# Kernel optimization log

Hardware: AMD Instinct MI355X
Metric: run time of the kernel (lower is better)

The kernel has to match this reference:

```python
import jax, jax.numpy as jnp
import numpy as np

VV = 100000   # value vocab
VP = 100000   # path vocab
VT = 50257    # tag vocab
E = 128       # embedding size
B = 2048      # batch of functions
N = 10        # rep_size (contexts per function)


def setup_inputs() -> dict:
    key = jax.random.key(0)
    ks = jax.random.split(key, 10)
    return {
        "value1_idx": jax.random.randint(ks[0], (B, N), 0, VV),
        "path_idx": jax.random.randint(ks[1], (B, N), 0, VP),
        "value2_idx": jax.random.randint(ks[2], (B, N), 0, VV),
        "value_emb": jax.random.normal(ks[3], (VV, E), jnp.float32) * 0.02,
        "path_emb": jax.random.normal(ks[4], (VP, E), jnp.float32) * 0.02,
        "tag_emb": jax.random.normal(ks[5], (VT, E), jnp.float32) * 0.02,
        "W_fc": jax.random.normal(ks[6], (3 * E, E), jnp.float32) * 0.02,
        "b_fc": jnp.zeros((E,), jnp.float32),
        "w_att": jax.random.normal(ks[7], (E,), jnp.float32) * 0.02,
        "b_att": jnp.zeros((), jnp.float32),
    }


def reference(value1_idx, path_idx, value2_idx, value_emb, path_emb, tag_emb,
              W_fc, b_fc, w_att, b_att):
    # Per-context embedding gathers: [B, N, E]
    v1 = value_emb[value1_idx]
    p = path_emb[path_idx]
    v2 = value_emb[value2_idx]
    ctx = jnp.concatenate([v1, p, v2], axis=-1)          # [B, N, 3E]
    c_tilde = jnp.tanh(ctx @ W_fc + b_fc)                # [B, N, E]
    # Attention pooling over the N contexts
    att = jax.nn.softmax(c_tilde @ w_att + b_att, axis=1)  # [B, N]
    v = jnp.einsum('bne,bn->be', c_tilde, att)           # [B, E]
    # Softmax classifier over all tags
    logits = v @ tag_emb.T                               # [B, VT]
    q = jax.nn.softmax(logits, axis=-1)
    return q
```

## Files before the change

### kernel.cpp

```cpp
#include <hip/hip_runtime.h>
#include <hip/hip_bf16.h>
#include <math.h>

#define VTAG 50257
#define EDIM 128
#define NREP 10
#define BFUNC 2048
#define NSTRIP 786
#define NPAD (NSTRIP * 64)

typedef __bf16 bf16x8 __attribute__((ext_vector_type(8)));
typedef float f32x4 __attribute__((ext_vector_type(4)));

__device__ __forceinline__ unsigned short f2bf(float x) {
    unsigned u = __float_as_uint(x);
    unsigned r = (u + 0x7fffu + ((u >> 16) & 1u)) >> 16;
    return (unsigned short)r;
}

__global__ __launch_bounds__(128) void k1_attn(
    const int* __restrict__ v1i, const int* __restrict__ pti,
    const int* __restrict__ v2i,
    const float* __restrict__ vemb, const float* __restrict__ pemb,
    const float* __restrict__ Wfc, const float* __restrict__ bfc,
    const float* __restrict__ watt, const float* __restrict__ batt,
    unsigned short* __restrict__ vbf)
{
    const int b = blockIdx.x;
    const int e = threadIdx.x;
    __shared__ float ctx[NREP][3 * EDIM];
    __shared__ float red[2][NREP];

    #pragma unroll
    for (int j = 0; j < 30; ++j) {
        int i = j * 128 + e;
        int n = i / 384;
        int c = i - n * 384;
        float val;
        if (c < 128)      val = vemb[(size_t)v1i[b * NREP + n] * EDIM + c];
        else if (c < 256) val = pemb[(size_t)pti[b * NREP + n] * EDIM + (c - 128)];
        else              val = vemb[(size_t)v2i[b * NREP + n] * EDIM + (c - 256)];
        ctx[n][c] = val;
    }
    __syncthreads();

    float acc[NREP];
    #pragma unroll
    for (int n = 0; n < NREP; ++n) acc[n] = 0.f;

    for (int k = 0; k < 384; k += 4) {
        float w0 = Wfc[(k + 0) * EDIM + e];
        float w1 = Wfc[(k + 1) * EDIM + e];
        float w2 = Wfc[(k + 2) * EDIM + e];
        float w3 = Wfc[(k + 3) * EDIM + e];
        #pragma unroll
        for (int n = 0; n < NREP; ++n) {
            float4 c4 = *(const float4*)&ctx[n][k];
            acc[n] = fmaf(c4.x, w0, acc[n]);
            acc[n] = fmaf(c4.y, w1, acc[n]);
            acc[n] = fmaf(c4.z, w2, acc[n]);
            acc[n] = fmaf(c4.w, w3, acc[n]);
        }
    }

    const float bias = bfc[e];
    const float we = watt[e];
    float ct[NREP];
    #pragma unroll
    for (int n = 0; n < NREP; ++n) ct[n] = tanhf(acc[n] + bias);

    const int wv = e >> 6, ln = e & 63;
    #pragma unroll
    for (int n = 0; n < NREP; ++n) {
        float p = ct[n] * we;
        p += __shfl_xor(p, 32);
        p += __shfl_xor(p, 16);
        p += __shfl_xor(p, 8);
        p += __shfl_xor(p, 4);
        p += __shfl_xor(p, 2);
        p += __shfl_xor(p, 1);
        if (ln == 0) red[wv][n] = p;
    }
    __syncthreads();

    const float batt0 = batt[0];
    float al[NREP];
    float m = -1e30f;
    #pragma unroll
    for (int n = 0; n < NREP; ++n) {
        al[n] = red[0][n] + red[1][n] + batt0;
        m = fmaxf(m, al[n]);
    }
    float s = 0.f;
    #pragma unroll
    for (int n = 0; n < NREP; ++n) { al[n] = __expf(al[n] - m); s += al[n]; }
    const float inv = 1.f / s;

    float v = 0.f;
    #pragma unroll
    for (int n = 0; n < NREP; ++n) v = fmaf(al[n] * inv, ct[n], v);

    vbf[b * EDIM + e] = f2bf(v);
}

__global__ __launch_bounds__(256) void k_conv_tag(
    const float* __restrict__ tag, unsigned short* __restrict__ tbf)
{
    size_t i = ((size_t)blockIdx.x * 256 + threadIdx.x) * 4;
    if (i >= (size_t)NPAD * EDIM) return;
    float4 x = make_float4(0.f, 0.f, 0.f, 0.f);
    if (i < (size_t)VTAG * EDIM) x = *(const float4*)(tag + i);
    ushort4 o;
    o.x = f2bf(x.x); o.y = f2bf(x.y); o.z = f2bf(x.z); o.w = f2bf(x.w);
    *(ushort4*)(tbf + i) = o;
}

__global__ __launch_bounds__(256) void k2_partial(
    const unsigned short* __restrict__ vbf, const unsigned short* __restrict__ tbf,
    float* __restrict__ psumT)
{
    const int wave = threadIdx.x >> 6;
    const int lane = threadIdx.x & 63;
    const int quad = lane >> 4;
    const int l16  = lane & 15;
    const int strip = blockIdx.y;
    const int n0 = strip * 64;
    const int rowbase = blockIdx.x * 128 + wave * 32;

    __shared__ float srow[128];

    const bf16x8* tb8 = (const bf16x8*)tbf;
    const bf16x8* vb8 = (const bf16x8*)vbf;

    bf16x8 bfrag[4][4];
    #pragma unroll
    for (int nt = 0; nt < 4; ++nt) {
        int col = n0 + nt * 16 + l16;
        const bf16x8* p = tb8 + (size_t)col * 16 + quad;
        #pragma unroll
        for (int ks = 0; ks < 4; ++ks) bfrag[nt][ks] = p[ks * 4];
    }
    bf16x8 afrag[2][4];
    #pragma unroll
    for (int mt = 0; mt < 2; ++mt) {
        int row = rowbase + mt * 16 + l16;
        const bf16x8* p = vb8 + (size_t)row * 16 + quad;
        #pragma unroll
        for (int ks = 0; ks < 4; ++ks) afrag[mt][ks] = p[ks * 4];
    }

    f32x4 acc[2][4];
    #pragma unroll
    for (int mt = 0; mt < 2; ++mt)
        #pragma unroll
        for (int nt = 0; nt < 4; ++nt) acc[mt][nt] = (f32x4){0.f, 0.f, 0.f, 0.f};

    #pragma unroll
    for (int ks = 0; ks < 4; ++ks)
        #pragma unroll
        for (int mt = 0; mt < 2; ++mt)
            #pragma unroll
            for (int nt = 0; nt < 4; ++nt)
                acc[mt][nt] = __builtin_amdgcn_mfma_f32_16x16x32_bf16(
                    afrag[mt][ks], bfrag[nt][ks], acc[mt][nt], 0, 0, 0);

    #pragma unroll
    for (int mt = 0; mt < 2; ++mt) {
        #pragma unroll
        for (int r = 0; r < 4; ++r) {
            float ls = 0.f;
            #pragma unroll
            for (int nt = 0; nt < 4; ++nt) {
                int col = n0 + nt * 16 + l16;
                if (col < VTAG) ls += __expf(acc[mt][nt][r]);
            }
            ls += __shfl_xor(ls, 1);
            ls += __shfl_xor(ls, 2);
            ls += __shfl_xor(ls, 4);
            ls += __shfl_xor(ls, 8);
            if (l16 == 0)
                srow[wave * 32 + mt * 16 + quad * 4 + r] = ls;
        }
    }
    __syncthreads();
    if (threadIdx.x < 128)
        psumT[(size_t)strip * BFUNC + blockIdx.x * 128 + threadIdx.x] =
            srow[threadIdx.x];
}

__global__ __launch_bounds__(256) void k3_reduce(
    const float* __restrict__ psumT, float* __restrict__ rowR)
{
    const int row = blockIdx.x * 256 + threadIdx.x;
    float s0 = 0.f, s1 = 0.f, s2 = 0.f, s3 = 0.f;
    int i = 0;
    for (; i + 4 <= NSTRIP; i += 4) {
        s0 += psumT[(size_t)(i + 0) * BFUNC + row];
        s1 += psumT[(size_t)(i + 1) * BFUNC + row];
        s2 += psumT[(size_t)(i + 2) * BFUNC + row];
        s3 += psumT[(size_t)(i + 3) * BFUNC + row];
    }
    for (; i < NSTRIP; ++i) s0 += psumT[(size_t)i * BFUNC + row];
    rowR[row] = 1.f / (s0 + s1 + s2 + s3);
}

__global__ __launch_bounds__(256) void k4_write(
    const unsigned short* __restrict__ vbf, const unsigned short* __restrict__ tbf,
    const float* __restrict__ rowR, float* __restrict__ out)
{
    const int wave = threadIdx.x >> 6;
    const int lane = threadIdx.x & 63;
    const int quad = lane >> 4;
    const int l16  = lane & 15;
    const int strip = blockIdx.y;
    const int n0 = strip * 64;
    const int rowbase = blockIdx.x * 128 + wave * 32;

    __shared__ float tile[128][65];

    const bf16x8* tb8 = (const bf16x8*)tbf;
    const bf16x8* vb8 = (const bf16x8*)vbf;

    float Rv[2][4];
    #pragma unroll
    for (int mt = 0; mt < 2; ++mt)
        #pragma unroll
        for (int r = 0; r < 4; ++r)
            Rv[mt][r] = rowR[rowbase + mt * 16 + quad * 4 + r];

    bf16x8 bfrag[4][4];
    #pragma unroll
    for (int nt = 0; nt < 4; ++nt) {
        int col = n0 + nt * 16 + l16;
        const bf16x8* p = tb8 + (size_t)col * 16 + quad;
        #pragma unroll
        for (int ks = 0; ks < 4; ++ks) bfrag[nt][ks] = p[ks * 4];
    }
    bf16x8 afrag[2][4];
    #pragma unroll
    for (int mt = 0; mt < 2; ++mt) {
        int row = rowbase + mt * 16 + l16;
        const bf16x8* p = vb8 + (size_t)row * 16 + quad;
        #pragma unroll
        for (int ks = 0; ks < 4; ++ks) afrag[mt][ks] = p[ks * 4];
    }

    f32x4 acc[2][4];
    #pragma unroll
    for (int mt = 0; mt < 2; ++mt)
        #pragma unroll
        for (int nt = 0; nt < 4; ++nt) acc[mt][nt] = (f32x4){0.f, 0.f, 0.f, 0.f};

    #pragma unroll
    for (int ks = 0; ks < 4; ++ks)
        #pragma unroll
        for (int mt = 0; mt < 2; ++mt)
            #pragma unroll
            for (int nt = 0; nt < 4; ++nt)
                acc[mt][nt] = __builtin_amdgcn_mfma_f32_16x16x32_bf16(
                    afrag[mt][ks], bfrag[nt][ks], acc[mt][nt], 0, 0, 0);

    #pragma unroll
    for (int mt = 0; mt < 2; ++mt) {
        #pragma unroll
        for (int r = 0; r < 4; ++r) {
            const int lrow = wave * 32 + mt * 16 + quad * 4 + r;
            const float R = Rv[mt][r];
            #pragma unroll
            for (int nt = 0; nt < 4; ++nt)
                tile[lrow][nt * 16 + l16] = __expf(acc[mt][nt][r]) * R;
        }
    }
    __syncthreads();

    const int ncol = (n0 + 64 <= VTAG) ? 64 : (VTAG - n0);
    const int gbase = blockIdx.x * 128;
    #pragma unroll 4
    for (int rr = 0; rr < 32; ++rr) {
        const int lrow = wave * 32 + rr;
        if (lane < ncol)
            out[(size_t)(gbase + lrow) * VTAG + n0 + lane] = tile[lrow][lane];
    }
}

extern "C" void kernel_launch(void* const* d_in, const int* in_sizes, int n_in,
                              void* d_out, int out_size, void* d_ws, size_t ws_size,
                              hipStream_t stream)
{
    const int*   v1i  = (const int*)d_in[0];
    const int*   pti  = (const int*)d_in[1];
    const int*   v2i  = (const int*)d_in[2];
    const float* vemb = (const float*)d_in[3];
    const float* pemb = (const float*)d_in[4];
    const float* temb = (const float*)d_in[5];
    const float* Wfc  = (const float*)d_in[6];
    const float* bfc  = (const float*)d_in[7];
    const float* watt = (const float*)d_in[8];
    const float* batt = (const float*)d_in[9];
    float* out = (float*)d_out;

    char* ws = (char*)d_ws;
    const size_t vbf_off  = 0;
    const size_t tbf_off  = vbf_off + 524288;
    const size_t psum_off = tbf_off + 12877824;
    const size_t rowr_off = psum_off + 6438912;

    unsigned short* vbf = (unsigned short*)(ws + vbf_off);
    unsigned short* tbf = (unsigned short*)(ws + tbf_off);
    float* psumT = (float*)(ws + psum_off);
    float* rowR  = (float*)(ws + rowr_off);

    hipLaunchKernelGGL(k1_attn, dim3(BFUNC), dim3(128), 0, stream,
                       v1i, pti, v2i, vemb, pemb, Wfc, bfc, watt, batt, vbf);
    hipLaunchKernelGGL(k_conv_tag, dim3((NPAD * EDIM / 4 + 255) / 256), dim3(256),
                       0, stream, temb, tbf);
    hipLaunchKernelGGL(k2_partial, dim3(BFUNC / 128, NSTRIP), dim3(256), 0, stream,
                       vbf, tbf, psumT);
    hipLaunchKernelGGL(k3_reduce, dim3(BFUNC / 256), dim3(256), 0, stream,
                       psumT, rowR);
    hipLaunchKernelGGL(k4_write, dim3(BFUNC / 128, NSTRIP), dim3(256), 0, stream,
                       vbf, tbf, rowR, out);
}
```

Before: 897.8 us.

## Store unnormalized exponentials in first pass and rescale in place

The first GEMM pass now writes the exponentiated logits straight to the output while it accumulates the per-strip row sums. The second GEMM plus exp pass is replaced by a simple elementwise kernel that multiplies each row by its reciprocal sum. This removes the duplicate matmul and exp work, but adds a full extra read and write of the large output. It also turns the first pass's stores into strided 16-float segments, which coalesce worse than the old shared-memory transpose. The reduction kernel is also unrolled to eight accumulators.

```diff
diff --git a/kernel.cpp b/kernel.cpp
--- a/kernel.cpp
+++ b/kernel.cpp
@@ -115,9 +115,9 @@
     *(ushort4*)(tbf + i) = o;
 }
 
-__global__ __launch_bounds__(256) void k2_partial(
+__global__ __launch_bounds__(256) void k2_expstore(
     const unsigned short* __restrict__ vbf, const unsigned short* __restrict__ tbf,
-    float* __restrict__ psumT)
+    float* __restrict__ out, float* __restrict__ psumT)
 {
     const int wave = threadIdx.x >> 6;
     const int lane = threadIdx.x & 63;
@@ -168,11 +168,16 @@
     for (int mt = 0; mt < 2; ++mt) {
         #pragma unroll
         for (int r = 0; r < 4; ++r) {
+            const int row = rowbase + mt * 16 + quad * 4 + r;
             float ls = 0.f;
             #pragma unroll
             for (int nt = 0; nt < 4; ++nt) {
                 int col = n0 + nt * 16 + l16;
-                if (col < VTAG) ls += __expf(acc[mt][nt][r]);
+                if (col < VTAG) {
+                    float ex = __expf(acc[mt][nt][r]);
+                    ls += ex;
+                    out[(size_t)row * VTAG + col] = ex;
+                }
             }
             ls += __shfl_xor(ls, 1);
             ls += __shfl_xor(ls, 2);
@@ -193,93 +198,42 @@
 {
     const int row = blockIdx.x * 256 + threadIdx.x;
     float s0 = 0.f, s1 = 0.f, s2 = 0.f, s3 = 0.f;
+    float s4 = 0.f, s5 = 0.f, s6 = 0.f, s7 = 0.f;
     int i = 0;
-    for (; i + 4 <= NSTRIP; i += 4) {
+    for (; i + 8 <= NSTRIP; i += 8) {
         s0 += psumT[(size_t)(i + 0) * BFUNC + row];
         s1 += psumT[(size_t)(i + 1) * BFUNC + row];
         s2 += psumT[(size_t)(i + 2) * BFUNC + row];
         s3 += psumT[(size_t)(i + 3) * BFUNC + row];
+        s4 += psumT[(size_t)(i + 4) * BFUNC + row];
+        s5 += psumT[(size_t)(i + 5) * BFUNC + row];
+        s6 += psumT[(size_t)(i + 6) * BFUNC + row];
+        s7 += psumT[(size_t)(i + 7) * BFUNC + row];
     }
     for (; i < NSTRIP; ++i) s0 += psumT[(size_t)i * BFUNC + row];
-    rowR[row] = 1.f / (s0 + s1 + s2 + s3);
-}
-
-__global__ __launch_bounds__(256) void k4_write(
-    const unsigned short* __restrict__ vbf, const unsigned short* __restrict__ tbf,
-    const float* __restrict__ rowR, float* __restrict__ out)
-{
-    const int wave = threadIdx.x >> 6;
-    const int lane = threadIdx.x & 63;
-    const int quad = lane >> 4;
-    const int l16  = lane & 15;
-    const int strip = blockIdx.y;
-    const int n0 = strip * 64;
-    const int rowbase = blockIdx.x * 128 + wave * 32;
-
-    __shared__ float tile[128][65];
-
-    const bf16x8* tb8 = (const bf16x8*)tbf;
-    const bf16x8* vb8 = (const bf16x8*)vbf;
-
-    float Rv[2][4];
-    #pragma unroll
-    for (int mt = 0; mt < 2; ++mt)
-        #pragma unroll
-        for (int r = 0; r < 4; ++r)
-            Rv[mt][r] = rowR[rowbase + mt * 16 + quad * 4 + r];
-
-    bf16x8 bfrag[4][4];
-    #pragma unroll
-    for (int nt = 0; nt < 4; ++nt) {
-        int col = n0 + nt * 16 + l16;
-        const bf16x8* p = tb8 + (size_t)col * 16 + quad;
-        #pragma unroll
-        for (int ks = 0; ks < 4; ++ks) bfrag[nt][ks] = p[ks * 4];
-    }
-    bf16x8 afrag[2][4];
-    #pragma unroll
-    for (int mt = 0; mt < 2; ++mt) {
-        int row = rowbase + mt * 16 + l16;
-        const bf16x8* p = vb8 + (size_t)row * 16 + quad;
-        #pragma unroll
-        for (int ks = 0; ks < 4; ++ks) afrag[mt][ks] = p[ks * 4];
-    }
-
-    f32x4 acc[2][4];
-    #pragma unroll
-    for (int mt = 0; mt < 2; ++mt)
-        #pragma unroll
-        for (int nt = 0; nt < 4; ++nt) acc[mt][nt] = (f32x4){0.f, 0.f, 0.f, 0.f};
-
-    #pragma unroll
-    for (int ks = 0; ks < 4; ++ks)
-        #pragma unroll
-        for (int mt = 0; mt < 2; ++mt)
-            #pragma unroll
-            for (int nt = 0; nt < 4; ++nt)
-                acc[mt][nt] = __builtin_amdgcn_mfma_f32_16x16x32_bf16(
-                    afrag[mt][ks], bfrag[nt][ks], acc[mt][nt], 0, 0, 0);
-
-    #pragma unroll
-    for (int mt = 0; mt < 2; ++mt) {
-        #pragma unroll
-        for (int r = 0; r < 4; ++r) {
-            const int lrow = wave * 32 + mt * 16 + quad * 4 + r;
-            const float R = Rv[mt][r];
-            #pragma unroll
-            for (int nt = 0; nt < 4; ++nt)
-                tile[lrow][nt * 16 + l16] = __expf(acc[mt][nt][r]) * R;
+    rowR[row] = 1.f / (((s0 + s1) + (s2 + s3)) + ((s4 + s5) + (s6 + s7)));
+}
+
+__global__ __launch_bounds__(256) void k4_scale(
+    float* __restrict__ out, const float* __restrict__ rowR)
+{
+    unsigned i0 = (blockIdx.x * 256u + threadIdx.x) * 4u;
+    const unsigned total = (unsigned)BFUNC * VTAG;
+    if (i0 >= total) return;
+    unsigned row = i0 / VTAG;
+    unsigned c = i0 - row * VTAG;
+    if (c + 4 <= VTAG) {
+        float R = rowR[row];
+        float4 x = *(float4*)(out + i0);
+        x.x *= R; x.y *= R; x.z *= R; x.w *= R;
+        *(float4*)(out + i0) = x;
+    } else {
+        #pragma unroll
+        for (int j = 0; j < 4; ++j) {
+            unsigned i = i0 + j;
+            unsigned r2 = i / VTAG;
+            out[i] *= rowR[r2];
         }
-    }
-    __syncthreads();
-
-    const int ncol = (n0 + 64 <= VTAG) ? 64 : (VTAG - n0);
-    const int gbase = blockIdx.x * 128;
-    #pragma unroll 4
-    for (int rr = 0; rr < 32; ++rr) {
-        const int lrow = wave * 32 + rr;
-        if (lane < ncol)
-            out[(size_t)(gbase + lrow) * VTAG + n0 + lane] = tile[lrow][lane];
     }
 }
 
@@ -314,10 +268,10 @@
                        v1i, pti, v2i, vemb, pemb, Wfc, bfc, watt, batt, vbf);
     hipLaunchKernelGGL(k_conv_tag, dim3((NPAD * EDIM / 4 + 255) / 256), dim3(256),
                        0, stream, temb, tbf);
-    hipLaunchKernelGGL(k2_partial, dim3(BFUNC / 128, NSTRIP), dim3(256), 0, stream,
-                       vbf, tbf, psumT);
+    hipLaunchKernelGGL(k2_expstore, dim3(BFUNC / 128, NSTRIP), dim3(256), 0, stream,
+                       vbf, tbf, out, psumT);
     hipLaunchKernelGGL(k3_reduce, dim3(BFUNC / 256), dim3(256), 0, stream,
                        psumT, rowR);
-    hipLaunchKernelGGL(k4_write, dim3(BFUNC / 128, NSTRIP), dim3(256), 0, stream,
-                       vbf, tbf, rowR, out);
-}
+    hipLaunchKernelGGL(k4_scale, dim3(((unsigned)BFUNC * VTAG / 4 + 255) / 256),
+                       dim3(256), 0, stream, out, rowR);
+}
```

After: 848.4 us. 5.5% less time.
